# Optimization experiments

Measured on AMD Instinct MI355X. Metric: run time of the kernel, lower is better.

The kernel has to match this reference:

```python
import jax, jax.numpy as jnp
import numpy as np

D_MODEL = 1024
N_EXPERTS = 16
D_FF = 4 * D_MODEL
B, T = 2, 2048


def setup_inputs() -> dict:
    key = jax.random.key(0)
    ks = jax.random.split(key, 6)
    s1 = 1.0 / np.sqrt(D_MODEL)
    s2 = 1.0 / np.sqrt(D_FF)
    return {
        "x": jax.random.normal(ks[0], (B, T, D_MODEL), dtype=jnp.float32),
        "W1": jax.random.normal(ks[1], (N_EXPERTS, D_MODEL, D_FF), dtype=jnp.float32) * s1,
        "b1": jnp.zeros((N_EXPERTS, D_FF), dtype=jnp.float32),
        "W2": jax.random.normal(ks[2], (N_EXPERTS, D_FF, D_MODEL), dtype=jnp.float32) * s2,
        "b2": jnp.zeros((N_EXPERTS, D_MODEL), dtype=jnp.float32),
        "Wg": jax.random.normal(ks[3], (D_MODEL, N_EXPERTS), dtype=jnp.float32) * s1,
        "k": 2,
    }


def reference(x, W1, b1, W2, b2, Wg, k):
    # Gating: [B,T,E] logits, top-k, softmax over selected logits
    gate_logits = jnp.einsum("btd,de->bte", x, Wg)
    topk_vals, topk_idx = jax.lax.top_k(gate_logits, k)      # [B,T,k]
    weights = jax.nn.softmax(topk_vals, axis=-1)             # [B,T,k]
    # Dense all-expert FFN (faithful to the original which computes every expert)
    h = jax.nn.swish(jnp.einsum("btd,edf->btef", x, W1) + b1)        # [B,T,E,4D]
    expert_out = jnp.einsum("btef,efd->bted", h, W2) + b2            # [B,T,E,D]
    # Gather top-k expert outputs per token and combine
    sel = jnp.take_along_axis(expert_out, topk_idx[..., None], axis=2)  # [B,T,k,D]
    return jnp.sum(sel * weights[..., None], axis=2)                    # [B,T,D]
```

## Files before the change

kernel.cpp:

```cpp
#include <hip/hip_runtime.h>
#include <cstdint>

#define D_MODEL 1024
#define N_EXP   16
#define D_FF    4096
#define NTOK    4096
#define NSEL    8192

typedef uint16_t u16;
typedef __bf16    bf16x8 __attribute__((ext_vector_type(8)));
typedef uint16_t  u16x8  __attribute__((ext_vector_type(8)));
typedef float     f32x4  __attribute__((ext_vector_type(4)));
typedef uint32_t  u32x2  __attribute__((ext_vector_type(2)));

__device__ __forceinline__ u16 f2bf(float x) {
    union { float f; uint32_t i; } c; c.f = x;
    uint32_t i = c.i + 0x7fffu + ((c.i >> 16) & 1u);
    return (u16)(i >> 16);
}

__device__ __forceinline__ uint32_t cvtpk(float lo, float hi) {
    uint32_t r;
    asm("v_cvt_pk_bf16_f32 %0, %1, %2" : "=v"(r) : "v"(lo), "v"(hi));
    return r;
}

#define ASYNC16(gp, lp) __builtin_amdgcn_global_load_lds( \
    (__attribute__((address_space(1))) void*)(gp),        \
    (__attribute__((address_space(3))) void*)(lp), 16, 0, 0)

__global__ void gate_kernel(const float* __restrict__ x, const float* __restrict__ Wg,
                            int* __restrict__ tok_idx, float* __restrict__ tok_w,
                            int* __restrict__ counts)
{
    const int lane = threadIdx.x & 63;
    const int t = blockIdx.x * 4 + (threadIdx.x >> 6);
    const float* xr = x + (size_t)t * D_MODEL;
    float acc[N_EXP];
    #pragma unroll
    for (int e = 0; e < N_EXP; e++) acc[e] = 0.f;
    for (int d = lane; d < D_MODEL; d += 64) {
        float xv = xr[d];
        const float* wr = Wg + d * N_EXP;
        #pragma unroll
        for (int e = 0; e < N_EXP; e++) acc[e] += xv * wr[e];
    }
    #pragma unroll
    for (int e = 0; e < N_EXP; e++) {
        float v = acc[e];
        #pragma unroll
        for (int o = 32; o > 0; o >>= 1) v += __shfl_xor(v, o, 64);
        acc[e] = v;
    }
    if (lane == 0) {
        int i0 = 0; float v0 = acc[0];
        #pragma unroll
        for (int e = 1; e < N_EXP; e++) if (acc[e] > v0) { v0 = acc[e]; i0 = e; }
        int i1 = (i0 == 0) ? 1 : 0; float v1 = -3.0e38f;
        #pragma unroll
        for (int e = 0; e < N_EXP; e++) if (e != i0 && acc[e] > v1) { v1 = acc[e]; i1 = e; }
        float e1  = __expf(v1 - v0);
        float inv = 1.f / (1.f + e1);
        tok_idx[2 * t] = i0;  tok_idx[2 * t + 1] = i1;
        tok_w[2 * t] = inv;   tok_w[2 * t + 1] = e1 * inv;
        atomicAdd(&counts[i0], 1);
        atomicAdd(&counts[i1], 1);
    }
}

__global__ void scan_kernel(const int* __restrict__ counts, int* __restrict__ offsets,
                            int* __restrict__ cursors)
{
    if (threadIdx.x == 0) {
        int s = 0;
        #pragma unroll
        for (int e = 0; e < N_EXP; e++) { offsets[e] = s; cursors[e] = s; s += counts[e]; }
        offsets[N_EXP] = s;
    }
}

__global__ void scatter_kernel(const int* __restrict__ tok_idx, const float* __restrict__ tok_w,
                               int* __restrict__ cursors, int* __restrict__ perm_token,
                               float* __restrict__ perm_w)
{
    const int t = blockIdx.x * 256 + threadIdx.x;
    #pragma unroll
    for (int j = 0; j < 2; j++) {
        int e = tok_idx[2 * t + j];
        int slot = atomicAdd(&cursors[e], 1);
        perm_token[slot] = t;
        perm_w[slot] = tok_w[2 * t + j];
    }
}

__global__ void gatherA_kernel(const float* __restrict__ x, const int* __restrict__ perm_token,
                               u16* __restrict__ Abf)
{
    const int slot = blockIdx.x;
    const int t = perm_token[slot];
    const float* src = x + (size_t)t * D_MODEL;
    u16* dst = Abf + (size_t)slot * D_MODEL;
    const int d = threadIdx.x * 4;
    f32x4 v = *(const f32x4*)(src + d);
    u32x2 o;
    o.x = cvtpk(v[0], v[1]);
    o.y = cvtpk(v[2], v[3]);
    *(u32x2*)(dst + d) = o;
}

template<bool SWISH, int KSPLIT>
__global__ __launch_bounds__(256, 3)
void gemm_kernel(const u16* __restrict__ A, const float* __restrict__ W,
                 const float* __restrict__ bias, const int* __restrict__ offsets,
                 const int* __restrict__ perm_token, const float* __restrict__ perm_w,
                 u16* __restrict__ Hout, float* __restrict__ Yout,
                 int K, int N)
{
    const int zz  = blockIdx.z;
    const int e   = zz & (N_EXP - 1);
    const int ks  = zz >> 4;
    const int off = offsets[e];
    const int cnt = offsets[e + 1] - off;
    const int m0  = blockIdx.y * 128;
    if (m0 >= cnt) return;
    const int n0  = blockIdx.x * 128;
    const int kbase  = ks * (K / KSPLIT);
    const int ksteps = (K / KSPLIT) / 32;

    __shared__ u16 Alds[2][128 * 32];
    __shared__ u16 Blds[2][128 * 32];

    const int tid  = threadIdx.x;
    const int lane = tid & 63;
    const int w    = tid >> 6;
    const int wm   = w & 1;
    const int wn   = w >> 1;

    const int arow = w * 16 + (lane >> 2);
    const int oA   = (lane & 3) ^ ((arow >> 1) & 3) ^ ((arow >> 3) & 3);
    int rA = m0 + arow;      if (rA > cnt - 1) rA = cnt - 1;
    int rB = m0 + arow + 64; if (rB > cnt - 1) rB = cnt - 1;
    const u16* aph0 = A + (size_t)(off + rA) * K + oA * 8;
    const u16* aph1 = A + (size_t)(off + rB) * K + oA * 8;

    const int fo = tid & 15;
    const int dp = tid >> 4;
    const int k0 = 2 * dp;
    const float* bbase = W + (size_t)e * K * N + n0 + fo * 8;
    const int koct = dp >> 2;
    const int kin  = k0 & 7;
    int boff[8];
    #pragma unroll
    for (int j = 0; j < 8; j++) {
        const int row = fo * 8 + j;
        const int oct = koct ^ (fo & 3) ^ ((j >> 1) & 3);
        boff[j] = row * 32 + oct * 8 + kin;
    }

    const int q = lane >> 4;
    int a_rd[4];
    #pragma unroll
    for (int mi = 0; mi < 4; mi++) {
        const int r   = wm * 64 + mi * 16 + (lane & 15);
        const int oct = q ^ ((r >> 1) & 3) ^ ((r >> 3) & 3);
        a_rd[mi] = r * 32 + oct * 8;
    }
    const int fbase = wn * 64 + (lane & 15);
    int b_rd[4];
    #pragma unroll
    for (int ni = 0; ni < 4; ni++) {
        const int f   = fbase + ni * 16;
        const int oct = q ^ ((f >> 1) & 3) ^ ((f >> 3) & 3);
        b_rd[ni] = f * 32 + oct * 8;
    }

    f32x4 acc[4][4] = {};

    {
        ASYNC16(aph0 + kbase, &Alds[0][w * 512]);
        ASYNC16(aph1 + kbase, &Alds[0][(w + 4) * 512]);
        const float* bp = bbase + (size_t)kbase * N;
        f32x4 w00 = *(const f32x4*)(bp + (size_t)k0 * N);
        f32x4 w01 = *(const f32x4*)(bp + (size_t)k0 * N + 4);
        f32x4 w10 = *(const f32x4*)(bp + (size_t)(k0 + 1) * N);
        f32x4 w11 = *(const f32x4*)(bp + (size_t)(k0 + 1) * N + 4);
        #pragma unroll
        for (int j = 0; j < 4; j++) *(uint32_t*)&Blds[0][boff[j]]     = cvtpk(w00[j], w10[j]);
        #pragma unroll
        for (int j = 0; j < 4; j++) *(uint32_t*)&Blds[0][boff[4 + j]] = cvtpk(w01[j], w11[j]);
    }
    __syncthreads();

    int cur = 0;
    for (int i = 0; i < ksteps; ++i) {
        const bool has_next = (i + 1 < ksteps);
        f32x4 w00, w01, w10, w11;
        if (has_next) {
            const int ktn = kbase + (i + 1) * 32;
            ASYNC16(aph0 + ktn, &Alds[cur ^ 1][w * 512]);
            ASYNC16(aph1 + ktn, &Alds[cur ^ 1][(w + 4) * 512]);
            const float* bp = bbase + (size_t)ktn * N;
            w00 = *(const f32x4*)(bp + (size_t)k0 * N);
            w01 = *(const f32x4*)(bp + (size_t)k0 * N + 4);
            w10 = *(const f32x4*)(bp + (size_t)(k0 + 1) * N);
            w11 = *(const f32x4*)(bp + (size_t)(k0 + 1) * N + 4);
        }

        u16x8 af[4], bfr[4];
        #pragma unroll
        for (int mi = 0; mi < 4; mi++) af[mi] = *(const u16x8*)(&Alds[cur][a_rd[mi]]);
        #pragma unroll
        for (int ni = 0; ni < 4; ni++) bfr[ni] = *(const u16x8*)(&Blds[cur][b_rd[ni]]);
        #pragma unroll
        for (int mi = 0; mi < 4; mi++)
            #pragma unroll
            for (int ni = 0; ni < 4; ni++)
                acc[mi][ni] = __builtin_amdgcn_mfma_f32_16x16x32_bf16(
                    __builtin_bit_cast(bf16x8, af[mi]),
                    __builtin_bit_cast(bf16x8, bfr[ni]),
                    acc[mi][ni], 0, 0, 0);

        if (has_next) {
            #pragma unroll
            for (int j = 0; j < 4; j++) *(uint32_t*)&Blds[cur ^ 1][boff[j]]     = cvtpk(w00[j], w10[j]);
            #pragma unroll
            for (int j = 0; j < 4; j++) *(uint32_t*)&Blds[cur ^ 1][boff[4 + j]] = cvtpk(w01[j], w11[j]);
            __syncthreads();
            cur ^= 1;
        }
    }

    const int rowq = (lane >> 4) * 4;
    #pragma unroll
    for (int mi = 0; mi < 4; mi++) {
        #pragma unroll
        for (int r = 0; r < 4; r++) {
            const int m = m0 + wm * 64 + mi * 16 + rowq + r;
            if (m < cnt) {
                const size_t gm = (size_t)(off + m);
                if constexpr (SWISH) {
                    #pragma unroll
                    for (int ni = 0; ni < 4; ni++) {
                        const int gn = n0 + fbase + ni * 16;
                        float c = acc[mi][ni][r] + bias[(size_t)e * N + gn];
                        float s = c / (1.f + __expf(-c));
                        Hout[gm * (size_t)N + gn] = f2bf(s);
                    }
                } else {
                    const int   tok = perm_token[gm];
                    const float pw  = perm_w[gm];
                    float* orow = Yout + (size_t)tok * N;
                    #pragma unroll
                    for (int ni = 0; ni < 4; ni++) {
                        const int gn = n0 + fbase + ni * 16;
                        float c = acc[mi][ni][r];
                        if (ks == 0) c += bias[(size_t)e * N + gn];
                        atomicAdd(&orow[gn], c * pw);
                    }
                }
            }
        }
    }
}

extern "C" void kernel_launch(void* const* d_in, const int* in_sizes, int n_in,
                              void* d_out, int out_size, void* d_ws, size_t ws_size,
                              hipStream_t stream)
{
    const float* x  = (const float*)d_in[0];
    const float* W1 = (const float*)d_in[1];
    const float* b1 = (const float*)d_in[2];
    const float* W2 = (const float*)d_in[3];
    const float* b2 = (const float*)d_in[4];
    const float* Wg = (const float*)d_in[5];

    char* ws = (char*)d_ws;
    int*   counts     = (int*)(ws);
    int*   offsets    = (int*)(ws + 64);
    int*   cursors    = (int*)(ws + 192);
    int*   tok_idx    = (int*)(ws + 256);
    float* tok_w      = (float*)(ws + 256 + 32768);
    int*   perm_token = (int*)(ws + 256 + 2 * 32768);
    float* perm_w     = (float*)(ws + 256 + 3 * 32768);
    u16*   h          = (u16*)(ws + 262144);
    u16*   Abf        = (u16*)(ws + 262144 + (size_t)NSEL * D_FF * 2);

    hipMemsetAsync(counts, 0, 64, stream);
    hipMemsetAsync(d_out, 0, out_size, stream);
    gate_kernel<<<dim3(NTOK / 4), dim3(256), 0, stream>>>(x, Wg, tok_idx, tok_w, counts);
    scan_kernel<<<dim3(1), dim3(64), 0, stream>>>(counts, offsets, cursors);
    scatter_kernel<<<dim3(NTOK / 256), dim3(256), 0, stream>>>(tok_idx, tok_w, cursors,
                                                               perm_token, perm_w);
    gatherA_kernel<<<dim3(NSEL), dim3(256), 0, stream>>>(x, perm_token, Abf);
    gemm_kernel<true, 1><<<dim3(32, 32, 16), dim3(256), 0, stream>>>(
        Abf, W1, b1, offsets, nullptr, nullptr, h, nullptr, D_MODEL, D_FF);
    gemm_kernel<false, 4><<<dim3(8, 32, 16 * 4), dim3(256), 0, stream>>>(
        h, W2, b2, offsets, perm_token, perm_w, nullptr, (float*)d_out, D_FF, D_MODEL);
}
```

Baseline: 942.5 us.

## Pre-transpose expert weights to bf16 and load B tiles asynchronously

Adds a transpose kernel that converts each expert's fp32 weight matrix into a transposed bf16 copy in workspace, run before each GEMM. This lets the GEMM stream B tiles with the same async 16-byte LDS copies used for A, replacing per-step fp32 register loads and bf16 conversion. The GEMMs also remap block indices with an interleaving swizzle, raise the occupancy hint to 4, and double the M grid dimension. The cost is an extra full read and write of both weight tensors on every call, and the workspace buffer is reused for W1t and W2t, which requires the first GEMM to finish before the second transpose runs.

New measurement: 1.025 ms. 1.09x slower.

```diff
diff --git a/kernel.cpp b/kernel.cpp
--- a/kernel.cpp
+++ b/kernel.cpp
@@ -108,22 +108,60 @@
     *(u32x2*)(dst + d) = o;
 }
 
+__global__ __launch_bounds__(256)
+void transpose_kernel(const float* __restrict__ W, u16* __restrict__ Wt, int K, int N)
+{
+    __shared__ u16 Tl[64 * 72];
+    const int e  = blockIdx.z;
+    const int n0 = blockIdx.x * 64, k0 = blockIdx.y * 64;
+    const int tid = threadIdx.x;
+    const float* src = W + (size_t)e * K * N + (size_t)k0 * N + n0;
+    u16* dst = Wt + (size_t)e * N * K + (size_t)n0 * K + k0;
+
+    const int kl = tid >> 4;
+    const int nl = (tid & 15) * 4;
+    #pragma unroll
+    for (int p = 0; p < 4; p++) {
+        const int kk = p * 16 + kl;
+        f32x4 v = *(const f32x4*)(src + (size_t)kk * N + nl);
+        #pragma unroll
+        for (int j = 0; j < 4; j++) Tl[(nl + j) * 72 + kk] = f2bf(v[j]);
+    }
+    __syncthreads();
+    const int nr = tid >> 3;
+    const int ks = (tid & 7) * 8;
+    #pragma unroll
+    for (int p = 0; p < 2; p++) {
+        const int nn = p * 32 + nr;
+        u16x8 o = *(const u16x8*)(&Tl[nn * 72 + ks]);
+        *(u16x8*)(dst + (size_t)nn * K + ks) = o;
+    }
+}
+
 template<bool SWISH, int KSPLIT>
-__global__ __launch_bounds__(256, 3)
-void gemm_kernel(const u16* __restrict__ A, const float* __restrict__ W,
+__global__ __launch_bounds__(256, 4)
+void gemm_kernel(const u16* __restrict__ A, const u16* __restrict__ Bt,
                  const float* __restrict__ bias, const int* __restrict__ offsets,
                  const int* __restrict__ perm_token, const float* __restrict__ perm_w,
                  u16* __restrict__ Hout, float* __restrict__ Yout,
                  int K, int N)
 {
-    const int zz  = blockIdx.z;
+    const int gx = gridDim.x, gy = gridDim.y;
+    const int L = blockIdx.x + gx * (blockIdx.y + gy * blockIdx.z);
+    const int total = gx * gy * gridDim.z;
+    const int wid = (L & 7) * (total >> 3) + (L >> 3);
+    const int nt  = wid % gx;
+    const int rem = wid / gx;
+    const int mt  = rem % gy;
+    const int zz  = rem / gy;
+
     const int e   = zz & (N_EXP - 1);
     const int ks  = zz >> 4;
     const int off = offsets[e];
     const int cnt = offsets[e + 1] - off;
-    const int m0  = blockIdx.y * 128;
+    const int m0  = mt * 128;
     if (m0 >= cnt) return;
-    const int n0  = blockIdx.x * 128;
+    const int n0  = nt * 128;
     const int kbase  = ks * (K / KSPLIT);
     const int ksteps = (K / KSPLIT) / 32;
 
@@ -136,26 +174,14 @@
     const int wm   = w & 1;
     const int wn   = w >> 1;
 
-    const int arow = w * 16 + (lane >> 2);
-    const int oA   = (lane & 3) ^ ((arow >> 1) & 3) ^ ((arow >> 3) & 3);
-    int rA = m0 + arow;      if (rA > cnt - 1) rA = cnt - 1;
-    int rB = m0 + arow + 64; if (rB > cnt - 1) rB = cnt - 1;
-    const u16* aph0 = A + (size_t)(off + rA) * K + oA * 8;
-    const u16* aph1 = A + (size_t)(off + rB) * K + oA * 8;
-
-    const int fo = tid & 15;
-    const int dp = tid >> 4;
-    const int k0 = 2 * dp;
-    const float* bbase = W + (size_t)e * K * N + n0 + fo * 8;
-    const int koct = dp >> 2;
-    const int kin  = k0 & 7;
-    int boff[8];
-    #pragma unroll
-    for (int j = 0; j < 8; j++) {
-        const int row = fo * 8 + j;
-        const int oct = koct ^ (fo & 3) ^ ((j >> 1) & 3);
-        boff[j] = row * 32 + oct * 8 + kin;
-    }
+    const int srow = w * 16 + (lane >> 2);
+    const int oS   = (lane & 3) ^ ((srow >> 1) & 3) ^ ((srow >> 3) & 3);
+    int rA = m0 + srow;      if (rA > cnt - 1) rA = cnt - 1;
+    int rB = m0 + srow + 64; if (rB > cnt - 1) rB = cnt - 1;
+    const u16* ap0 = A + (size_t)(off + rA) * K + oS * 8;
+    const u16* ap1 = A + (size_t)(off + rB) * K + oS * 8;
+    const u16* bp0 = Bt + ((size_t)e * N + n0 + srow) * K + oS * 8;
+    const u16* bp1 = Bt + ((size_t)e * N + n0 + srow + 64) * K + oS * 8;
 
     const int q = lane >> 4;
     int a_rd[4];
@@ -176,34 +202,21 @@
 
     f32x4 acc[4][4] = {};
 
-    {
-        ASYNC16(aph0 + kbase, &Alds[0][w * 512]);
-        ASYNC16(aph1 + kbase, &Alds[0][(w + 4) * 512]);
-        const float* bp = bbase + (size_t)kbase * N;
-        f32x4 w00 = *(const f32x4*)(bp + (size_t)k0 * N);
-        f32x4 w01 = *(const f32x4*)(bp + (size_t)k0 * N + 4);
-        f32x4 w10 = *(const f32x4*)(bp + (size_t)(k0 + 1) * N);
-        f32x4 w11 = *(const f32x4*)(bp + (size_t)(k0 + 1) * N + 4);
-        #pragma unroll
-        for (int j = 0; j < 4; j++) *(uint32_t*)&Blds[0][boff[j]]     = cvtpk(w00[j], w10[j]);
-        #pragma unroll
-        for (int j = 0; j < 4; j++) *(uint32_t*)&Blds[0][boff[4 + j]] = cvtpk(w01[j], w11[j]);
-    }
+    ASYNC16(ap0 + kbase, &Alds[0][w * 512]);
+    ASYNC16(ap1 + kbase, &Alds[0][(w + 4) * 512]);
+    ASYNC16(bp0 + kbase, &Blds[0][w * 512]);
+    ASYNC16(bp1 + kbase, &Blds[0][(w + 4) * 512]);
     __syncthreads();
 
     int cur = 0;
     for (int i = 0; i < ksteps; ++i) {
         const bool has_next = (i + 1 < ksteps);
-        f32x4 w00, w01, w10, w11;
         if (has_next) {
             const int ktn = kbase + (i + 1) * 32;
-            ASYNC16(aph0 + ktn, &Alds[cur ^ 1][w * 512]);
-            ASYNC16(aph1 + ktn, &Alds[cur ^ 1][(w + 4) * 512]);
-            const float* bp = bbase + (size_t)ktn * N;
-            w00 = *(const f32x4*)(bp + (size_t)k0 * N);
-            w01 = *(const f32x4*)(bp + (size_t)k0 * N + 4);
-            w10 = *(const f32x4*)(bp + (size_t)(k0 + 1) * N);
-            w11 = *(const f32x4*)(bp + (size_t)(k0 + 1) * N + 4);
+            ASYNC16(ap0 + ktn, &Alds[cur ^ 1][w * 512]);
+            ASYNC16(ap1 + ktn, &Alds[cur ^ 1][(w + 4) * 512]);
+            ASYNC16(bp0 + ktn, &Blds[cur ^ 1][w * 512]);
+            ASYNC16(bp1 + ktn, &Blds[cur ^ 1][(w + 4) * 512]);
         }
 
         u16x8 af[4], bfr[4];
@@ -221,10 +234,6 @@
                     acc[mi][ni], 0, 0, 0);
 
         if (has_next) {
-            #pragma unroll
-            for (int j = 0; j < 4; j++) *(uint32_t*)&Blds[cur ^ 1][boff[j]]     = cvtpk(w00[j], w10[j]);
-            #pragma unroll
-            for (int j = 0; j < 4; j++) *(uint32_t*)&Blds[cur ^ 1][boff[4 + j]] = cvtpk(w01[j], w11[j]);
             __syncthreads();
             cur ^= 1;
         }
@@ -282,18 +291,30 @@
     float* tok_w      = (float*)(ws + 256 + 32768);
     int*   perm_token = (int*)(ws + 256 + 2 * 32768);
     float* perm_w     = (float*)(ws + 256 + 3 * 32768);
-    u16*   h          = (u16*)(ws + 262144);
-    u16*   Abf        = (u16*)(ws + 262144 + (size_t)NSEL * D_FF * 2);
+    u16*   h   = (u16*)(ws + 262144);
+    u16*   Abf = (u16*)(ws + 262144 + (size_t)NSEL * D_FF * 2);
+    u16*   W1t = (u16*)(ws + 262144 + (size_t)NSEL * D_FF * 2
+                              + (size_t)NSEL * D_MODEL * 2);
+    u16*   W2t = W1t;
 
     hipMemsetAsync(counts, 0, 64, stream);
     hipMemsetAsync(d_out, 0, out_size, stream);
+
+    transpose_kernel<<<dim3(D_FF / 64, D_MODEL / 64, N_EXP), dim3(256), 0, stream>>>(
+        W1, W1t, D_MODEL, D_FF);
+
     gate_kernel<<<dim3(NTOK / 4), dim3(256), 0, stream>>>(x, Wg, tok_idx, tok_w, counts);
     scan_kernel<<<dim3(1), dim3(64), 0, stream>>>(counts, offsets, cursors);
     scatter_kernel<<<dim3(NTOK / 256), dim3(256), 0, stream>>>(tok_idx, tok_w, cursors,
                                                                perm_token, perm_w);
     gatherA_kernel<<<dim3(NSEL), dim3(256), 0, stream>>>(x, perm_token, Abf);
-    gemm_kernel<true, 1><<<dim3(32, 32, 16), dim3(256), 0, stream>>>(
-        Abf, W1, b1, offsets, nullptr, nullptr, h, nullptr, D_MODEL, D_FF);
-    gemm_kernel<false, 4><<<dim3(8, 32, 16 * 4), dim3(256), 0, stream>>>(
-        h, W2, b2, offsets, perm_token, perm_w, nullptr, (float*)d_out, D_FF, D_MODEL);
-}
+
+    gemm_kernel<true, 1><<<dim3(32, 64, 16), dim3(256), 0, stream>>>(
+        Abf, W1t, b1, offsets, nullptr, nullptr, h, nullptr, D_MODEL, D_FF);
+
+    transpose_kernel<<<dim3(D_MODEL / 64, D_FF / 64, N_EXP), dim3(256), 0, stream>>>(
+        W2, W2t, D_FF, D_MODEL);
+
+    gemm_kernel<false, 4><<<dim3(8, 64, 16 * 4), dim3(256), 0, stream>>>(
+        h, W2t, b2, offsets, perm_token, perm_w, nullptr, (float*)d_out, D_FF, D_MODEL);
+}
```
